# Optimization experiments

Measured on AMD Instinct MI355X. Metric: run time of the kernel, lower is better.

## Reference

```python
import jax, jax.numpy as jnp
import numpy as np

P = 4096          # n_patch (64x64 grid)
S = 64            # grid side
L = 9             # 9-neighbor window
E = 34            # attention embed dim (32 hidden + 2 coords)
H = 32            # hidden size
N_OBS = 10
N_PRED = 50


def _neighbor_flat_idx():
    idx = np.arange(P)
    r, c = idx // S, idx % S
    off = np.array([[-1,-1],[-1,0],[-1,1],[0,-1],[0,0],[0,1],[1,-1],[1,0],[1,1]])
    nr = (r[:, None] + off[:, 0]).reshape(S, S, L)
    nc = (c[:, None] + off[:, 1]).reshape(S, S, L)
    # boundary shift (as in the torch module)
    nr[0] += 1; nr[-1] -= 1
    nc[:, 0] += 1; nc[:, -1] -= 1
    return jnp.asarray((nr * S + nc).reshape(P, L))  # [P, 9] into patch dim


def _patch_label(B):
    coords = jnp.arange(S, dtype=jnp.float32) / S
    pl = jnp.stack(jnp.meshgrid(coords, coords, indexing='ij'), -1).reshape(P, 2)
    return jnp.broadcast_to(pl[:, None, :], (P, B, 2))  # [P, B, 2]


def setup_inputs() -> dict:
    key = jax.random.key(0)
    ks = jax.random.split(key, 8)
    s = 0.1
    return {
        'x': jax.random.normal(ks[0], (N_OBS, 2 * P, H), jnp.float32),
        'W_x2h': jax.random.normal(ks[1], (H, H), jnp.float32) * s,
        'b_x2h': jnp.zeros((H,), jnp.float32),
        'W_h2h': jax.random.normal(ks[2], (H, H), jnp.float32) * s,
        'b_h2h': jnp.zeros((H,), jnp.float32),
        'W_fc2': jax.random.normal(ks[3], (H, H), jnp.float32) * s,
        'b_fc2': jnp.zeros((H,), jnp.float32),
        'ln_g': jnp.ones((H,), jnp.float32),
        'ln_b': jnp.zeros((H,), jnp.float32),
        'W_fcsa': jax.random.normal(ks[4], (H, E), jnp.float32) * s,
        'b_fcsa': jnp.zeros((H,), jnp.float32),
        'W_in': jax.random.normal(ks[5], (3 * E, E), jnp.float32) * s,
        'b_in': jnp.zeros((3 * E,), jnp.float32),
        'W_out': jax.random.normal(ks[6], (E, E), jnp.float32) * s,
        'b_out': jnp.zeros((E,), jnp.float32),
    }


def reference(x, W_x2h, b_x2h, W_h2h, b_h2h, W_fc2, b_fc2, ln_g, ln_b,
              W_fcsa, b_fcsa, W_in, b_in, W_out, b_out):
    B = x.shape[1] // P
    N = B * P
    nbr = _neighbor_flat_idx()
    pl = _patch_label(B)

    def layernorm(y):
        mu = jnp.mean(y, -1, keepdims=True)
        var = jnp.mean((y - mu) ** 2, -1, keepdims=True)
        return (y - mu) * jax.lax.rsqrt(var + 1e-5) * ln_g + ln_b

    def mha(xa):  # [L, N, E] self-attention, 1 head
        qkv = xa @ W_in.T + b_in
        q, k, v = jnp.split(qkv, 3, axis=-1)
        scores = jnp.einsum('lne,mne->nlm', q, k) / jnp.sqrt(jnp.float32(E))
        w = jax.nn.softmax(scores, axis=-1)
        o = jnp.einsum('nlm,mne->lne', w, v)
        return o @ W_out.T + b_out

    def step(h, inp):
        h = jnp.tanh(inp @ W_x2h.T + b_x2h + h @ W_h2h.T + b_h2h)  # [N, H]
        hb = jnp.transpose(h.reshape(B, P, H), (1, 0, 2))          # [P, B, H]
        qin = jnp.concatenate([hb, pl], -1)                        # [P, B, E]
        nq = qin[nbr]                                              # [P, 9, B, E]
        xa = jnp.transpose(nq, (1, 2, 0, 3)).reshape(L, N, E)      # [9, N, E]
        ao = mha(xa)[4]                                            # center, [N, E]
        h = h + ao @ W_fcsa.T + b_fcsa
        pred = layernorm(h @ W_fc2.T + b_fc2)
        return h, pred

    h0 = jnp.zeros((N, H), x.dtype)
    h, preds_obs = jax.lax.scan(step, h0, x)                       # [10, N, H]

    def step_pred(carry, _):
        h, p = carry
        h, pnew = step(h, p)
        return (h, pnew), pnew

    _, preds_fut = jax.lax.scan(step_pred, (h, preds_obs[-1]), None,
                                length=N_PRED - 1)                 # [49, N, H]
    return jnp.concatenate([preds_obs, preds_fut], 0)              # [59, N, H]
```

## Files before the change

### kernel.cpp

```cpp
#include <hip/hip_runtime.h>

#define NROWS 8192
#define RPB   64
#define TPB   1024
#define NBLK  128

#define OFF_W1   0
#define OFF_W2   1024
#define OFF_WIN  2048
#define OFF_WFC2 5516
#define OFF_M    6540
#define OFF_B12  7628
#define OFF_BIN  7660
#define OFF_B2   7762
#define OFF_BFC2 7794
#define OFF_LNG  7826
#define OFF_LNB  7858
#define OFF_QKV0 8192
#define QKVN     (NROWS*102)
#define OFF_QKV1 (OFF_QKV0 + QKVN)
#define OFF_HNEW (OFF_QKV1 + QKVN)

__global__ __launch_bounds__(256) void setup_kernel(
    const float* __restrict__ W_x2h, const float* __restrict__ b_x2h,
    const float* __restrict__ W_h2h, const float* __restrict__ b_h2h,
    const float* __restrict__ W_fc2, const float* __restrict__ b_fc2,
    const float* __restrict__ ln_g,  const float* __restrict__ ln_b,
    const float* __restrict__ W_fcsa,const float* __restrict__ b_fcsa,
    const float* __restrict__ W_in,  const float* __restrict__ b_in,
    const float* __restrict__ W_out, const float* __restrict__ b_out,
    float* __restrict__ ws)
{
  int t = blockIdx.x*blockDim.x + threadIdx.x;
  int stride = gridDim.x*blockDim.x;
  for (int i=t;i<1024;i+=stride) ws[OFF_W1+i]   = W_x2h[i];
  for (int i=t;i<1024;i+=stride) ws[OFF_W2+i]   = W_h2h[i];
  for (int i=t;i<3468;i+=stride) ws[OFF_WIN+i]  = W_in[i];
  for (int i=t;i<1024;i+=stride) ws[OFF_WFC2+i] = W_fc2[i];
  for (int i=t;i<32;i+=stride)   ws[OFF_B12+i]  = b_x2h[i] + b_h2h[i];
  for (int i=t;i<102;i+=stride)  ws[OFF_BIN+i]  = b_in[i];
  for (int i=t;i<32;i+=stride)   ws[OFF_BFC2+i] = b_fc2[i];
  for (int i=t;i<32;i+=stride)   ws[OFF_LNG+i]  = ln_g[i];
  for (int i=t;i<32;i+=stride)   ws[OFF_LNB+i]  = ln_b[i];
  for (int idx=t; idx<1088; idx+=stride) {
    int j = idx/34, f = idx - j*34;
    float acc = 0.f;
    for (int e=0;e<34;++e)
      acc += W_fcsa[j*34+e] * W_out[e*34+f];
    ws[OFF_M+idx] = acc;
  }
  for (int j=t;j<32;j+=stride){
    float acc = b_fcsa[j];
    for (int e=0;e<34;++e) acc += W_fcsa[j*34+e] * b_out[e];
    ws[OFF_B2+j] = acc;
  }
}

__global__ __launch_bounds__(TPB) void step_kernel(
    const float* __restrict__ ws,
    const float* __restrict__ qkvR,
    float* __restrict__ qkvW,
    float* __restrict__ hnewG,
    const float* __restrict__ x,
    float* __restrict__ out,
    int stepB, int stepA)
{
  const float* W1f   = ws + OFF_W1;
  const float* W2f   = ws + OFF_W2;
  const float* Winf  = ws + OFF_WIN;
  const float* Wfc2f = ws + OFF_WFC2;
  const float* Mf    = ws + OFF_M;
  const float* b12f  = ws + OFF_B12;
  const float* binf  = ws + OFF_BIN;
  const float* b2f   = ws + OFF_B2;
  const float* bfc2f = ws + OFF_BFC2;
  const float* lngf  = ws + OFF_LNG;
  const float* lnbf  = ws + OFF_LNB;

  __shared__ float sS[RPB][13];
  __shared__ float sO[RPB][35];
  __shared__ float sHp[RPB][33];
  __shared__ float sG[RPB][33];
  __shared__ float sPred[RPB][33];
  __shared__ float sHn[RPB][33];
  __shared__ float sX[RPB][33];

  const int tid = threadIdx.x;
  const int lr  = tid & 63;
  const int wu  = __builtin_amdgcn_readfirstlane(tid >> 6);
  const int base= blockIdx.x * RPB;
  const int r   = base + lr;
  const int b   = r >> 12;
  const int p   = r & 4095;
  const int gr  = p >> 6, gc = p & 63;
  const int br  = (gr < 1) ? 1 : ((gr > 62) ? 62 : gr);
  const int bc  = (gc < 1) ? 1 : ((gc > 62) ? 62 : gc);

  if (stepB >= 0) {
    if (wu < 9) {
      const int qrow = (b<<12) + (br<<6) + bc;
      const int m  = wu;
      const int dr = m/3 - 1, dc = m - (m/3)*3 - 1;
      const int nr_ = (b<<12) + ((br+dr)<<6) + (bc+dc);
      float acc = 0.f;
      #pragma unroll
      for (int e=0;e<34;++e)
        acc += qkvR[(size_t)e*NROWS + qrow] * qkvR[(size_t)(34+e)*NROWS + nr_];
      sS[lr][m] = acc * 0.1714985851425088f;
    } else {
      const int tid2 = (wu-9)*64 + lr;
      #pragma unroll
      for (int it=0; it<5; ++it) {
        int idx = tid2 + it*448;
        if (idx < 2048) {
          int j = idx >> 6, rr = idx & 63;
          sHp[rr][j] = hnewG[(size_t)j*NROWS + base + rr];
        }
      }
    }
    __syncthreads();
    {
      float sc[9]; float mx = -1e30f;
      #pragma unroll
      for (int m=0;m<9;++m){ sc[m]=sS[lr][m]; mx=fmaxf(mx,sc[m]); }
      float sum=0.f;
      #pragma unroll
      for (int m=0;m<9;++m){ sc[m]=__expf(sc[m]-mx); sum+=sc[m]; }
      float inv = 1.f/sum;
      float o0=0.f, o1=0.f, o2=0.f;
      const bool e2ok = (wu < 2);
      #pragma unroll
      for (int m=0;m<9;++m){
        int dr = m/3 - 1, dc = m - (m/3)*3 - 1;
        int nr_ = (b<<12) + ((br+dr)<<6) + (bc+dc);
        float wm = sc[m]*inv;
        o0 += wm * qkvR[(size_t)(68+wu)   *NROWS + nr_];
        o1 += wm * qkvR[(size_t)(68+wu+16)*NROWS + nr_];
        if (e2ok) o2 += wm * qkvR[(size_t)(68+wu+32)*NROWS + nr_];
      }
      sO[lr][wu]    = o0;
      sO[lr][wu+16] = o1;
      if (e2ok) sO[lr][wu+32] = o2;
    }
    __syncthreads();
    {
      const int j0 = wu*2;
      float a0 = b2f[j0], a1 = b2f[j0+1];
      #pragma unroll
      for (int e=0;e<34;++e){
        float ov = sO[lr][e];
        a0 += ov * Mf[j0*34+e];
        a1 += ov * Mf[(j0+1)*34+e];
      }
      sHp[lr][j0]   += a0;
      sHp[lr][j0+1] += a1;
    }
    __syncthreads();
    {
      const int j0 = wu*2;
      float g0 = bfc2f[j0], g1 = bfc2f[j0+1];
      #pragma unroll
      for (int i=0;i<32;++i){
        float hv = sHp[lr][i];
        g0 += hv * Wfc2f[j0*32+i];
        g1 += hv * Wfc2f[(j0+1)*32+i];
      }
      sG[lr][j0]=g0; sG[lr][j0+1]=g1;
    }
    __syncthreads();
    {
      float mu=0.f;
      #pragma unroll
      for (int i=0;i<32;++i) mu += sG[lr][i];
      mu *= 0.03125f;
      float var=0.f;
      #pragma unroll
      for (int i=0;i<32;++i){ float d=sG[lr][i]-mu; var += d*d; }
      var *= 0.03125f;
      float rs = rsqrtf(var + 1e-5f);
      const int j0 = wu*2;
      sPred[lr][j0]   = (sG[lr][j0]  -mu)*rs*lngf[j0]   + lnbf[j0];
      sPred[lr][j0+1] = (sG[lr][j0+1]-mu)*rs*lngf[j0+1] + lnbf[j0+1];
    }
    __syncthreads();
    {
      size_t obase = ((size_t)stepB*NROWS + base)*32;
      #pragma unroll
      for (int it=0; it<2; ++it){
        int idx = tid + it*TPB;
        out[obase + idx] = sPred[idx>>5][idx&31];
      }
    }
  } else {
    const int j0 = wu*2;
    sHp[lr][j0]=0.f; sHp[lr][j0+1]=0.f;
    __syncthreads();
  }

  if (stepA >= 0) {
    if (stepA < 10) {
      size_t xbase = ((size_t)stepA*NROWS + base)*32;
      #pragma unroll
      for (int it=0; it<2; ++it){
        int idx = tid + it*TPB;
        sX[idx>>5][idx&31] = x[xbase + idx];
      }
    }
    __syncthreads();
    const int j0 = wu*2;
    float a0=b12f[j0], a1=b12f[j0+1];
    if (stepA < 10) {
      #pragma unroll
      for (int i=0;i<32;++i){
        float xv=sX[lr][i], hv=sHp[lr][i];
        a0 += xv*W1f[j0*32+i]     + hv*W2f[j0*32+i];
        a1 += xv*W1f[(j0+1)*32+i] + hv*W2f[(j0+1)*32+i];
      }
    } else {
      #pragma unroll
      for (int i=0;i<32;++i){
        float xv=sPred[lr][i], hv=sHp[lr][i];
        a0 += xv*W1f[j0*32+i]     + hv*W2f[j0*32+i];
        a1 += xv*W1f[(j0+1)*32+i] + hv*W2f[(j0+1)*32+i];
      }
    }
    {
      float t0 = tanhf(a0), t1 = tanhf(a1);
      sHn[lr][j0]=t0; sHn[lr][j0+1]=t1;
      hnewG[(size_t)j0*NROWS + r]=t0;
      hnewG[(size_t)(j0+1)*NROWS + r]=t1;
    }
    __syncthreads();
    float hn[32];
    #pragma unroll
    for (int f=0;f<32;++f) hn[f]=sHn[lr][f];
    const float pl0 = gr*0.015625f, pl1 = gc*0.015625f;
    #pragma unroll
    for (int k=0;k<7;++k){
      int e = wu + 16*k;
      if (e < 102) {
        float acc = binf[e];
        #pragma unroll
        for (int f=0;f<32;++f) acc += hn[f]*Winf[e*34+f];
        acc += pl0*Winf[e*34+32] + pl1*Winf[e*34+33];
        qkvW[(size_t)e*NROWS + r] = acc;
      }
    }
  }
}

extern "C" void kernel_launch(void* const* d_in, const int* in_sizes, int n_in,
                              void* d_out, int out_size, void* d_ws, size_t ws_size,
                              hipStream_t stream) {
  const float* x     = (const float*)d_in[0];
  const float* W_x2h = (const float*)d_in[1];
  const float* b_x2h = (const float*)d_in[2];
  const float* W_h2h = (const float*)d_in[3];
  const float* b_h2h = (const float*)d_in[4];
  const float* W_fc2 = (const float*)d_in[5];
  const float* b_fc2 = (const float*)d_in[6];
  const float* ln_g  = (const float*)d_in[7];
  const float* ln_b  = (const float*)d_in[8];
  const float* W_fcsa= (const float*)d_in[9];
  const float* b_fcsa= (const float*)d_in[10];
  const float* W_in  = (const float*)d_in[11];
  const float* b_in  = (const float*)d_in[12];
  const float* W_out = (const float*)d_in[13];
  const float* b_out = (const float*)d_in[14];
  float* ws = (float*)d_ws;
  float* out = (float*)d_out;

  setup_kernel<<<8, 256, 0, stream>>>(W_x2h,b_x2h,W_h2h,b_h2h,W_fc2,b_fc2,ln_g,ln_b,
                                      W_fcsa,b_fcsa,W_in,b_in,W_out,b_out, ws);
  for (int i=0;i<60;++i){
    int stepB = i-1;
    int stepA = (i<=58)? i : -1;
    const float* qR = ws + OFF_QKV0 + (size_t)((i+1)&1)*QKVN;
    float*       qW = ws + OFF_QKV0 + (size_t)(i&1)*QKVN;
    step_kernel<<<NBLK, TPB, 0, stream>>>(ws, qR, qW, ws+OFF_HNEW, x, out, stepB, stepA);
  }
}
```

Measured before the change: 1.008 ms.

## Fuse all time steps into one persistent kernel with grid barrier

Replaces the 60 per-step kernel launches with a single persistent kernel that loops over steps and synchronises blocks through an atomic-counter grid barrier in workspace. Each block now stages its three neighbour rows of QKV into shared memory before the attention stage, and the hidden state stays in shared memory instead of going through a global buffer. This removes launch gaps and repeated global gathers, at the cost of a spin-wait barrier that assumes all 128 blocks are co-resident and has a poll cap that could silently break synchronisation.

```diff
diff --git a/kernel.cpp b/kernel.cpp
--- a/kernel.cpp
+++ b/kernel.cpp
@@ -16,10 +16,10 @@
 #define OFF_BFC2 7794
 #define OFF_LNG  7826
 #define OFF_LNB  7858
+#define OFF_BAR  7904
 #define OFF_QKV0 8192
 #define QKVN     (NROWS*102)
 #define OFF_QKV1 (OFF_QKV0 + QKVN)
-#define OFF_HNEW (OFF_QKV1 + QKVN)
 
 __global__ __launch_bounds__(256) void setup_kernel(
     const float* __restrict__ W_x2h, const float* __restrict__ b_x2h,
@@ -42,6 +42,7 @@
   for (int i=t;i<32;i+=stride)   ws[OFF_BFC2+i] = b_fc2[i];
   for (int i=t;i<32;i+=stride)   ws[OFF_LNG+i]  = ln_g[i];
   for (int i=t;i<32;i+=stride)   ws[OFF_LNB+i]  = ln_b[i];
+  for (int i=t;i<64;i+=stride)   ((int*)(ws+OFF_BAR))[i] = 0;
   for (int idx=t; idx<1088; idx+=stride) {
     int j = idx/34, f = idx - j*34;
     float acc = 0.f;
@@ -56,14 +57,10 @@
   }
 }
 
-__global__ __launch_bounds__(TPB) void step_kernel(
-    const float* __restrict__ ws,
-    const float* __restrict__ qkvR,
-    float* __restrict__ qkvW,
-    float* __restrict__ hnewG,
+__global__ __launch_bounds__(TPB) void fused_kernel(
+    float* __restrict__ ws,
     const float* __restrict__ x,
-    float* __restrict__ out,
-    int stepB, int stepA)
+    float* __restrict__ out)
 {
   const float* W1f   = ws + OFF_W1;
   const float* W2f   = ws + OFF_W2;
@@ -76,7 +73,11 @@
   const float* bfc2f = ws + OFF_BFC2;
   const float* lngf  = ws + OFF_LNG;
   const float* lnbf  = ws + OFF_LNB;
-
+  int*  bar = (int*)(ws + OFF_BAR);
+  float* q0 = ws + OFF_QKV0;
+  float* q1 = ws + OFF_QKV1;
+
+  __shared__ float sQKV[3][102][64];
   __shared__ float sS[RPB][13];
   __shared__ float sO[RPB][35];
   __shared__ float sHp[RPB][33];
@@ -90,161 +91,182 @@
   const int wu  = __builtin_amdgcn_readfirstlane(tid >> 6);
   const int base= blockIdx.x * RPB;
   const int r   = base + lr;
-  const int b   = r >> 12;
-  const int p   = r & 4095;
-  const int gr  = p >> 6, gc = p & 63;
-  const int br  = (gr < 1) ? 1 : ((gr > 62) ? 62 : gr);
-  const int bc  = (gc < 1) ? 1 : ((gc > 62) ? 62 : gc);
-
-  if (stepB >= 0) {
-    if (wu < 9) {
-      const int qrow = (b<<12) + (br<<6) + bc;
-      const int m  = wu;
-      const int dr = m/3 - 1, dc = m - (m/3)*3 - 1;
-      const int nr_ = (b<<12) + ((br+dr)<<6) + (bc+dc);
-      float acc = 0.f;
-      #pragma unroll
-      for (int e=0;e<34;++e)
-        acc += qkvR[(size_t)e*NROWS + qrow] * qkvR[(size_t)(34+e)*NROWS + nr_];
-      sS[lr][m] = acc * 0.1714985851425088f;
+  const int bb  = base >> 12;
+  const int grb = (base & 4095) >> 6;
+  const int brb = (grb < 1) ? 1 : ((grb > 62) ? 62 : grb);
+  const int bc  = (lr < 1) ? 1 : ((lr > 62) ? 62 : lr);
+  const int rb0 = (bb << 12) + ((brb - 1) << 6);
+
+  for (int i = 0; i < 60; ++i) {
+    const int stepB = i - 1;
+    const int stepA = (i <= 58) ? i : -1;
+    const float* qR = ((i + 1) & 1) ? q1 : q0;
+    float*       qW = (i & 1) ? q1 : q0;
+
+    if (stepB >= 0) {
+      #pragma unroll
+      for (int k = 0; k < 20; ++k) {
+        int chunk = wu + 16*k;
+        if (chunk < 306) {
+          int drp = chunk / 102;
+          int e   = chunk - drp*102;
+          sQKV[drp][e][lr] = qR[(size_t)e*NROWS + rb0 + (drp<<6) + lr];
+        }
+      }
     } else {
-      const int tid2 = (wu-9)*64 + lr;
-      #pragma unroll
-      for (int it=0; it<5; ++it) {
-        int idx = tid2 + it*448;
-        if (idx < 2048) {
-          int j = idx >> 6, rr = idx & 63;
-          sHp[rr][j] = hnewG[(size_t)j*NROWS + base + rr];
-        }
-      }
-    }
-    __syncthreads();
-    {
-      float sc[9]; float mx = -1e30f;
-      #pragma unroll
-      for (int m=0;m<9;++m){ sc[m]=sS[lr][m]; mx=fmaxf(mx,sc[m]); }
-      float sum=0.f;
-      #pragma unroll
-      for (int m=0;m<9;++m){ sc[m]=__expf(sc[m]-mx); sum+=sc[m]; }
-      float inv = 1.f/sum;
-      float o0=0.f, o1=0.f, o2=0.f;
-      const bool e2ok = (wu < 2);
-      #pragma unroll
-      for (int m=0;m<9;++m){
-        int dr = m/3 - 1, dc = m - (m/3)*3 - 1;
-        int nr_ = (b<<12) + ((br+dr)<<6) + (bc+dc);
-        float wm = sc[m]*inv;
-        o0 += wm * qkvR[(size_t)(68+wu)   *NROWS + nr_];
-        o1 += wm * qkvR[(size_t)(68+wu+16)*NROWS + nr_];
-        if (e2ok) o2 += wm * qkvR[(size_t)(68+wu+32)*NROWS + nr_];
-      }
-      sO[lr][wu]    = o0;
-      sO[lr][wu+16] = o1;
-      if (e2ok) sO[lr][wu+32] = o2;
-    }
-    __syncthreads();
-    {
-      const int j0 = wu*2;
-      float a0 = b2f[j0], a1 = b2f[j0+1];
-      #pragma unroll
-      for (int e=0;e<34;++e){
-        float ov = sO[lr][e];
-        a0 += ov * Mf[j0*34+e];
-        a1 += ov * Mf[(j0+1)*34+e];
-      }
-      sHp[lr][j0]   += a0;
-      sHp[lr][j0+1] += a1;
-    }
-    __syncthreads();
-    {
-      const int j0 = wu*2;
-      float g0 = bfc2f[j0], g1 = bfc2f[j0+1];
-      #pragma unroll
-      for (int i=0;i<32;++i){
-        float hv = sHp[lr][i];
-        g0 += hv * Wfc2f[j0*32+i];
-        g1 += hv * Wfc2f[(j0+1)*32+i];
-      }
-      sG[lr][j0]=g0; sG[lr][j0+1]=g1;
-    }
-    __syncthreads();
-    {
-      float mu=0.f;
-      #pragma unroll
-      for (int i=0;i<32;++i) mu += sG[lr][i];
-      mu *= 0.03125f;
-      float var=0.f;
-      #pragma unroll
-      for (int i=0;i<32;++i){ float d=sG[lr][i]-mu; var += d*d; }
-      var *= 0.03125f;
-      float rs = rsqrtf(var + 1e-5f);
-      const int j0 = wu*2;
-      sPred[lr][j0]   = (sG[lr][j0]  -mu)*rs*lngf[j0]   + lnbf[j0];
-      sPred[lr][j0+1] = (sG[lr][j0+1]-mu)*rs*lngf[j0+1] + lnbf[j0+1];
-    }
-    __syncthreads();
-    {
-      size_t obase = ((size_t)stepB*NROWS + base)*32;
-      #pragma unroll
-      for (int it=0; it<2; ++it){
-        int idx = tid + it*TPB;
-        out[obase + idx] = sPred[idx>>5][idx&31];
-      }
-    }
-  } else {
-    const int j0 = wu*2;
-    sHp[lr][j0]=0.f; sHp[lr][j0+1]=0.f;
-    __syncthreads();
-  }
-
-  if (stepA >= 0) {
-    if (stepA < 10) {
+      sHp[lr][2*wu] = 0.f; sHp[lr][2*wu+1] = 0.f;
+    }
+    if (stepA >= 0 && stepA < 10) {
       size_t xbase = ((size_t)stepA*NROWS + base)*32;
       #pragma unroll
-      for (int it=0; it<2; ++it){
+      for (int it = 0; it < 2; ++it) {
         int idx = tid + it*TPB;
         sX[idx>>5][idx&31] = x[xbase + idx];
       }
     }
     __syncthreads();
-    const int j0 = wu*2;
-    float a0=b12f[j0], a1=b12f[j0+1];
-    if (stepA < 10) {
-      #pragma unroll
-      for (int i=0;i<32;++i){
-        float xv=sX[lr][i], hv=sHp[lr][i];
-        a0 += xv*W1f[j0*32+i]     + hv*W2f[j0*32+i];
-        a1 += xv*W1f[(j0+1)*32+i] + hv*W2f[(j0+1)*32+i];
-      }
-    } else {
-      #pragma unroll
-      for (int i=0;i<32;++i){
-        float xv=sPred[lr][i], hv=sHp[lr][i];
-        a0 += xv*W1f[j0*32+i]     + hv*W2f[j0*32+i];
-        a1 += xv*W1f[(j0+1)*32+i] + hv*W2f[(j0+1)*32+i];
-      }
-    }
-    {
-      float t0 = tanhf(a0), t1 = tanhf(a1);
-      sHn[lr][j0]=t0; sHn[lr][j0+1]=t1;
-      hnewG[(size_t)j0*NROWS + r]=t0;
-      hnewG[(size_t)(j0+1)*NROWS + r]=t1;
-    }
-    __syncthreads();
-    float hn[32];
-    #pragma unroll
-    for (int f=0;f<32;++f) hn[f]=sHn[lr][f];
-    const float pl0 = gr*0.015625f, pl1 = gc*0.015625f;
-    #pragma unroll
-    for (int k=0;k<7;++k){
-      int e = wu + 16*k;
-      if (e < 102) {
-        float acc = binf[e];
-        #pragma unroll
-        for (int f=0;f<32;++f) acc += hn[f]*Winf[e*34+f];
-        acc += pl0*Winf[e*34+32] + pl1*Winf[e*34+33];
-        qkvW[(size_t)e*NROWS + r] = acc;
-      }
+
+    if (stepB >= 0) {
+      if (wu < 9) {
+        const int slot = wu / 3;
+        const int col  = bc + (wu - slot*3 - 1);
+        float acc = 0.f;
+        #pragma unroll
+        for (int e = 0; e < 34; ++e)
+          acc += sQKV[1][e][bc] * sQKV[slot][34+e][col];
+        sS[lr][wu] = acc * 0.1714985851425088f;
+      }
+      __syncthreads();
+      {
+        float sc[9]; float mx = -1e30f;
+        #pragma unroll
+        for (int m=0;m<9;++m){ sc[m]=sS[lr][m]; mx=fmaxf(mx,sc[m]); }
+        float sum=0.f;
+        #pragma unroll
+        for (int m=0;m<9;++m){ sc[m]=__expf(sc[m]-mx); sum+=sc[m]; }
+        float inv = 1.f/sum;
+        float o0=0.f, o1=0.f, o2=0.f;
+        const bool e2ok = (wu < 2);
+        #pragma unroll
+        for (int m=0;m<9;++m){
+          const int slot = m/3;
+          const int col  = bc + (m - slot*3 - 1);
+          float wm = sc[m]*inv;
+          o0 += wm * sQKV[slot][68+wu][col];
+          o1 += wm * sQKV[slot][84+wu][col];
+          if (e2ok) o2 += wm * sQKV[slot][100+wu][col];
+        }
+        sO[lr][wu]    = o0;
+        sO[lr][wu+16] = o1;
+        if (e2ok) sO[lr][wu+32] = o2;
+      }
+      __syncthreads();
+      {
+        const int j0 = wu*2;
+        float a0 = b2f[j0], a1 = b2f[j0+1];
+        #pragma unroll
+        for (int e=0;e<34;++e){
+          float ov = sO[lr][e];
+          a0 += ov * Mf[j0*34+e];
+          a1 += ov * Mf[(j0+1)*34+e];
+        }
+        sHp[lr][j0]   = sHn[lr][j0]   + a0;
+        sHp[lr][j0+1] = sHn[lr][j0+1] + a1;
+      }
+      __syncthreads();
+      {
+        const int j0 = wu*2;
+        float g0 = bfc2f[j0], g1 = bfc2f[j0+1];
+        #pragma unroll
+        for (int ii=0;ii<32;++ii){
+          float hv = sHp[lr][ii];
+          g0 += hv * Wfc2f[j0*32+ii];
+          g1 += hv * Wfc2f[(j0+1)*32+ii];
+        }
+        sG[lr][j0]=g0; sG[lr][j0+1]=g1;
+      }
+      __syncthreads();
+      {
+        float mu=0.f;
+        #pragma unroll
+        for (int ii=0;ii<32;++ii) mu += sG[lr][ii];
+        mu *= 0.03125f;
+        float var=0.f;
+        #pragma unroll
+        for (int ii=0;ii<32;++ii){ float d=sG[lr][ii]-mu; var += d*d; }
+        var *= 0.03125f;
+        float rs = rsqrtf(var + 1e-5f);
+        const int j0 = wu*2;
+        sPred[lr][j0]   = (sG[lr][j0]  -mu)*rs*lngf[j0]   + lnbf[j0];
+        sPred[lr][j0+1] = (sG[lr][j0+1]-mu)*rs*lngf[j0+1] + lnbf[j0+1];
+      }
+      __syncthreads();
+      {
+        size_t obase = ((size_t)stepB*NROWS + base)*32;
+        #pragma unroll
+        for (int it=0; it<2; ++it){
+          int idx = tid + it*TPB;
+          out[obase + idx] = sPred[idx>>5][idx&31];
+        }
+      }
+    }
+
+    if (stepA >= 0) {
+      const int j0 = wu*2;
+      float a0=b12f[j0], a1=b12f[j0+1];
+      if (stepA < 10) {
+        #pragma unroll
+        for (int ii=0;ii<32;++ii){
+          float xv=sX[lr][ii], hv=sHp[lr][ii];
+          a0 += xv*W1f[j0*32+ii]     + hv*W2f[j0*32+ii];
+          a1 += xv*W1f[(j0+1)*32+ii] + hv*W2f[(j0+1)*32+ii];
+        }
+      } else {
+        #pragma unroll
+        for (int ii=0;ii<32;++ii){
+          float xv=sPred[lr][ii], hv=sHp[lr][ii];
+          a0 += xv*W1f[j0*32+ii]     + hv*W2f[j0*32+ii];
+          a1 += xv*W1f[(j0+1)*32+ii] + hv*W2f[(j0+1)*32+ii];
+        }
+      }
+      {
+        float t0 = tanhf(a0), t1 = tanhf(a1);
+        sHn[lr][j0]=t0; sHn[lr][j0+1]=t1;
+      }
+      __syncthreads();
+      float hn[32];
+      #pragma unroll
+      for (int f=0;f<32;++f) hn[f]=sHn[lr][f];
+      const float pl0 = grb*0.015625f, pl1 = lr*0.015625f;
+      #pragma unroll
+      for (int k=0;k<7;++k){
+        int e = wu + 16*k;
+        if (e < 102) {
+          float acc = binf[e];
+          #pragma unroll
+          for (int f=0;f<32;++f) acc += hn[f]*Winf[e*34+f];
+          acc += pl0*Winf[e*34+32] + pl1*Winf[e*34+33];
+          qW[(size_t)e*NROWS + r] = acc;
+        }
+      }
+    }
+
+    if (i < 59) {
+      __syncthreads();
+      if (tid == 0) {
+        __threadfence();
+        __hip_atomic_fetch_add(&bar[i], 1, __ATOMIC_RELAXED,
+                               __HIP_MEMORY_SCOPE_AGENT);
+        int polls = 0;
+        while (__hip_atomic_load(&bar[i], __ATOMIC_RELAXED,
+                                 __HIP_MEMORY_SCOPE_AGENT) < NBLK
+               && polls < (1<<21)) {
+          __builtin_amdgcn_s_sleep(2);
+          ++polls;
+        }
+        __threadfence();
+      }
+      __syncthreads();
     }
   }
 }
@@ -272,11 +294,5 @@
 
   setup_kernel<<<8, 256, 0, stream>>>(W_x2h,b_x2h,W_h2h,b_h2h,W_fc2,b_fc2,ln_g,ln_b,
                                       W_fcsa,b_fcsa,W_in,b_in,W_out,b_out, ws);
-  for (int i=0;i<60;++i){
-    int stepB = i-1;
-    int stepA = (i<=58)? i : -1;
-    const float* qR = ws + OFF_QKV0 + (size_t)((i+1)&1)*QKVN;
-    float*       qW = ws + OFF_QKV0 + (size_t)(i&1)*QKVN;
-    step_kernel<<<NBLK, TPB, 0, stream>>>(ws, qR, qW, ws+OFF_HNEW, x, out, stepB, stepA);
-  }
+  fused_kernel<<<NBLK, TPB, 0, stream>>>(ws, x, out);
 }
```

Measured after the change: 2.365 ms. +134.8%, slower.

## Stage weights in LDS, halve rows per block, merge initial loads

Applied to the files above, without the earlier changes.

Rows per block go from 64 to 32 and the block count doubles. Each thread now computes one output column instead of two. All weight matrices and biases are staged into shared memory at kernel start instead of being read from global memory inside the inner loops. The loads of x, the previous hidden state and the attention scores now sit in one phase behind a single barrier. The weight staging adds per-block load work, and the no-stepB branch now has to issue matching dummy barriers.

```diff
diff --git a/kernel.cpp b/kernel.cpp
--- a/kernel.cpp
+++ b/kernel.cpp
@@ -1,9 +1,9 @@
 #include <hip/hip_runtime.h>
 
 #define NROWS 8192
-#define RPB   64
+#define RPB   32
 #define TPB   1024
-#define NBLK  128
+#define NBLK  256
 
 #define OFF_W1   0
 #define OFF_W2   1024
@@ -65,18 +65,10 @@
     float* __restrict__ out,
     int stepB, int stepA)
 {
-  const float* W1f   = ws + OFF_W1;
-  const float* W2f   = ws + OFF_W2;
-  const float* Winf  = ws + OFF_WIN;
-  const float* Wfc2f = ws + OFF_WFC2;
-  const float* Mf    = ws + OFF_M;
-  const float* b12f  = ws + OFF_B12;
-  const float* binf  = ws + OFF_BIN;
-  const float* b2f   = ws + OFF_B2;
-  const float* bfc2f = ws + OFF_BFC2;
-  const float* lngf  = ws + OFF_LNG;
-  const float* lnbf  = ws + OFF_LNB;
-
+  __shared__ float sW1[32][32], sW2[32][32], sWfc2[32][32];
+  __shared__ float sM[32][36];
+  __shared__ float sWin[102][36];
+  __shared__ float sB12[32], sBin[102], sB2[32], sBfc2[32], sLng[32], sLnb[32];
   __shared__ float sS[RPB][13];
   __shared__ float sO[RPB][35];
   __shared__ float sHp[RPB][33];
@@ -85,165 +77,145 @@
   __shared__ float sHn[RPB][33];
   __shared__ float sX[RPB][33];
 
-  const int tid = threadIdx.x;
-  const int lr  = tid & 63;
-  const int wu  = __builtin_amdgcn_readfirstlane(tid >> 6);
-  const int base= blockIdx.x * RPB;
-  const int r   = base + lr;
-  const int b   = r >> 12;
-  const int p   = r & 4095;
-  const int gr  = p >> 6, gc = p & 63;
-  const int br  = (gr < 1) ? 1 : ((gr > 62) ? 62 : gr);
-  const int bc  = (gc < 1) ? 1 : ((gc > 62) ? 62 : gc);
-
+  const int tid  = threadIdx.x;
+  const int lr2  = tid & 31;
+  const int slot = tid >> 5;
+  const int base = blockIdx.x * RPB;
+  const int r2   = base + lr2;
+  const int b    = base >> 12;
+  const int p    = base & 4095;
+  const int gr   = p >> 6;
+  const int gc0  = p & 63;
+  const int c    = gc0 + lr2;
+  const int br   = (gr < 1) ? 1 : ((gr > 62) ? 62 : gr);
+  const int bc   = (c  < 1) ? 1 : ((c  > 62) ? 62 : c);
+
+  {
+    sW1  [tid>>5][tid&31] = ws[OFF_W1  +tid];
+    sW2  [tid>>5][tid&31] = ws[OFF_W2  +tid];
+    sWfc2[tid>>5][tid&31] = ws[OFF_WFC2+tid];
+    for (int idx=tid; idx<1088; idx+=TPB){ int j=idx/34, e=idx-j*34; sM[j][e]=ws[OFF_M+idx]; }
+    for (int idx=tid; idx<3468; idx+=TPB){ int e=idx/34, f=idx-e*34; sWin[e][f]=ws[OFF_WIN+idx]; }
+    if (tid < 102)                    sBin [tid]     = ws[OFF_BIN +tid];
+    else if (tid>=128 && tid<160)     sB12 [tid-128] = ws[OFF_B12 +tid-128];
+    else if (tid>=160 && tid<192)     sB2  [tid-160] = ws[OFF_B2  +tid-160];
+    else if (tid>=192 && tid<224)     sBfc2[tid-192] = ws[OFF_BFC2+tid-192];
+    else if (tid>=224 && tid<256)     sLng [tid-224] = ws[OFF_LNG +tid-224];
+    else if (tid>=256 && tid<288)     sLnb [tid-256] = ws[OFF_LNB +tid-256];
+  }
+  if (stepA >= 0 && stepA < 10) {
+    size_t xbase = ((size_t)stepA*NROWS + base)*32;
+    sX[tid>>5][tid&31] = x[xbase + tid];
+  }
   if (stepB >= 0) {
-    if (wu < 9) {
+    if (slot >= 16) {
+      const int j0 = (slot-16)*2;
+      sHp[lr2][j0]   = hnewG[(size_t)j0    *NROWS + r2];
+      sHp[lr2][j0+1] = hnewG[(size_t)(j0+1)*NROWS + r2];
+    } else if (slot < 9) {
+      const int m  = slot;
+      const int dr = m/3 - 1, dc = m - (m/3)*3 - 1;
       const int qrow = (b<<12) + (br<<6) + bc;
-      const int m  = wu;
-      const int dr = m/3 - 1, dc = m - (m/3)*3 - 1;
-      const int nr_ = (b<<12) + ((br+dr)<<6) + (bc+dc);
+      const int nr_  = (b<<12) + ((br+dr)<<6) + (bc+dc);
       float acc = 0.f;
       #pragma unroll
       for (int e=0;e<34;++e)
         acc += qkvR[(size_t)e*NROWS + qrow] * qkvR[(size_t)(34+e)*NROWS + nr_];
-      sS[lr][m] = acc * 0.1714985851425088f;
-    } else {
-      const int tid2 = (wu-9)*64 + lr;
-      #pragma unroll
-      for (int it=0; it<5; ++it) {
-        int idx = tid2 + it*448;
-        if (idx < 2048) {
-          int j = idx >> 6, rr = idx & 63;
-          sHp[rr][j] = hnewG[(size_t)j*NROWS + base + rr];
-        }
-      }
-    }
-    __syncthreads();
+      sS[lr2][m] = acc * 0.1714985851425088f;
+    }
+  } else {
+    sHp[lr2][slot] = 0.f;
+  }
+  __syncthreads();
+
+  if (stepB >= 0) {
     {
       float sc[9]; float mx = -1e30f;
       #pragma unroll
-      for (int m=0;m<9;++m){ sc[m]=sS[lr][m]; mx=fmaxf(mx,sc[m]); }
+      for (int m=0;m<9;++m){ sc[m]=sS[lr2][m]; mx=fmaxf(mx,sc[m]); }
       float sum=0.f;
       #pragma unroll
       for (int m=0;m<9;++m){ sc[m]=__expf(sc[m]-mx); sum+=sc[m]; }
       float inv = 1.f/sum;
-      float o0=0.f, o1=0.f, o2=0.f;
-      const bool e2ok = (wu < 2);
+      float o0=0.f, o1=0.f;
+      const bool e2ok = (slot < 2);
       #pragma unroll
       for (int m=0;m<9;++m){
         int dr = m/3 - 1, dc = m - (m/3)*3 - 1;
         int nr_ = (b<<12) + ((br+dr)<<6) + (bc+dc);
         float wm = sc[m]*inv;
-        o0 += wm * qkvR[(size_t)(68+wu)   *NROWS + nr_];
-        o1 += wm * qkvR[(size_t)(68+wu+16)*NROWS + nr_];
-        if (e2ok) o2 += wm * qkvR[(size_t)(68+wu+32)*NROWS + nr_];
+        o0 += wm * qkvR[(size_t)(68+slot)*NROWS + nr_];
+        if (e2ok) o1 += wm * qkvR[(size_t)(100+slot)*NROWS + nr_];
       }
-      sO[lr][wu]    = o0;
-      sO[lr][wu+16] = o1;
-      if (e2ok) sO[lr][wu+32] = o2;
-    }
-    __syncthreads();
-    {
-      const int j0 = wu*2;
-      float a0 = b2f[j0], a1 = b2f[j0+1];
-      #pragma unroll
-      for (int e=0;e<34;++e){
-        float ov = sO[lr][e];
-        a0 += ov * Mf[j0*34+e];
-        a1 += ov * Mf[(j0+1)*34+e];
-      }
-      sHp[lr][j0]   += a0;
-      sHp[lr][j0+1] += a1;
-    }
-    __syncthreads();
-    {
-      const int j0 = wu*2;
-      float g0 = bfc2f[j0], g1 = bfc2f[j0+1];
-      #pragma unroll
-      for (int i=0;i<32;++i){
-        float hv = sHp[lr][i];
-        g0 += hv * Wfc2f[j0*32+i];
-        g1 += hv * Wfc2f[(j0+1)*32+i];
-      }
-      sG[lr][j0]=g0; sG[lr][j0+1]=g1;
+      sO[lr2][slot] = o0;
+      if (e2ok) sO[lr2][32+slot] = o1;
+    }
+    __syncthreads();
+    {
+      float a = sB2[slot];
+      #pragma unroll
+      for (int e=0;e<34;++e) a += sO[lr2][e] * sM[slot][e];
+      sHp[lr2][slot] += a;
+    }
+    __syncthreads();
+    {
+      float g = sBfc2[slot];
+      #pragma unroll
+      for (int i=0;i<32;++i) g += sHp[lr2][i] * sWfc2[slot][i];
+      sG[lr2][slot] = g;
     }
     __syncthreads();
     {
       float mu=0.f;
       #pragma unroll
-      for (int i=0;i<32;++i) mu += sG[lr][i];
+      for (int i=0;i<32;++i) mu += sG[lr2][i];
       mu *= 0.03125f;
       float var=0.f;
       #pragma unroll
-      for (int i=0;i<32;++i){ float d=sG[lr][i]-mu; var += d*d; }
+      for (int i=0;i<32;++i){ float d=sG[lr2][i]-mu; var += d*d; }
       var *= 0.03125f;
       float rs = rsqrtf(var + 1e-5f);
-      const int j0 = wu*2;
-      sPred[lr][j0]   = (sG[lr][j0]  -mu)*rs*lngf[j0]   + lnbf[j0];
-      sPred[lr][j0+1] = (sG[lr][j0+1]-mu)*rs*lngf[j0+1] + lnbf[j0+1];
+      sPred[lr2][slot] = (sG[lr2][slot]-mu)*rs*sLng[slot] + sLnb[slot];
     }
     __syncthreads();
     {
       size_t obase = ((size_t)stepB*NROWS + base)*32;
-      #pragma unroll
-      for (int it=0; it<2; ++it){
-        int idx = tid + it*TPB;
-        out[obase + idx] = sPred[idx>>5][idx&31];
-      }
+      out[obase + tid] = sPred[tid>>5][tid&31];
     }
   } else {
-    const int j0 = wu*2;
-    sHp[lr][j0]=0.f; sHp[lr][j0+1]=0.f;
-    __syncthreads();
+    __syncthreads(); __syncthreads(); __syncthreads(); __syncthreads();
   }
 
   if (stepA >= 0) {
+    float a = sB12[slot];
     if (stepA < 10) {
-      size_t xbase = ((size_t)stepA*NROWS + base)*32;
-      #pragma unroll
-      for (int it=0; it<2; ++it){
-        int idx = tid + it*TPB;
-        sX[idx>>5][idx&31] = x[xbase + idx];
-      }
-    }
-    __syncthreads();
-    const int j0 = wu*2;
-    float a0=b12f[j0], a1=b12f[j0+1];
-    if (stepA < 10) {
-      #pragma unroll
-      for (int i=0;i<32;++i){
-        float xv=sX[lr][i], hv=sHp[lr][i];
-        a0 += xv*W1f[j0*32+i]     + hv*W2f[j0*32+i];
-        a1 += xv*W1f[(j0+1)*32+i] + hv*W2f[(j0+1)*32+i];
-      }
+      #pragma unroll
+      for (int i=0;i<32;++i)
+        a += sX[lr2][i]*sW1[slot][i] + sHp[lr2][i]*sW2[slot][i];
     } else {
       #pragma unroll
-      for (int i=0;i<32;++i){
-        float xv=sPred[lr][i], hv=sHp[lr][i];
-        a0 += xv*W1f[j0*32+i]     + hv*W2f[j0*32+i];
-        a1 += xv*W1f[(j0+1)*32+i] + hv*W2f[(j0+1)*32+i];
-      }
-    }
-    {
-      float t0 = tanhf(a0), t1 = tanhf(a1);
-      sHn[lr][j0]=t0; sHn[lr][j0+1]=t1;
-      hnewG[(size_t)j0*NROWS + r]=t0;
-      hnewG[(size_t)(j0+1)*NROWS + r]=t1;
+      for (int i=0;i<32;++i)
+        a += sPred[lr2][i]*sW1[slot][i] + sHp[lr2][i]*sW2[slot][i];
+    }
+    {
+      float t0 = tanhf(a);
+      sHn[lr2][slot] = t0;
+      hnewG[(size_t)slot*NROWS + r2] = t0;
     }
     __syncthreads();
     float hn[32];
     #pragma unroll
-    for (int f=0;f<32;++f) hn[f]=sHn[lr][f];
-    const float pl0 = gr*0.015625f, pl1 = gc*0.015625f;
+    for (int f=0;f<32;++f) hn[f]=sHn[lr2][f];
+    const float pl0 = gr*0.015625f, pl1 = c*0.015625f;
     #pragma unroll
-    for (int k=0;k<7;++k){
-      int e = wu + 16*k;
+    for (int k=0;k<4;++k){
+      int e = slot + 32*k;
       if (e < 102) {
-        float acc = binf[e];
+        float acc = sBin[e];
         #pragma unroll
-        for (int f=0;f<32;++f) acc += hn[f]*Winf[e*34+f];
-        acc += pl0*Winf[e*34+32] + pl1*Winf[e*34+33];
-        qkvW[(size_t)e*NROWS + r] = acc;
+        for (int f=0;f<32;++f) acc += hn[f]*sWin[e][f];
+        acc += pl0*sWin[e][32] + pl1*sWin[e][33];
+        qkvW[(size_t)e*NROWS + r2] = acc;
       }
     }
   }
```

Result: faster. 962.6 us (-4.5%).
